# Kernel optimization log

Measured on AMD Instinct MI355X. Metric: run time of the kernel, lower is better.

Reference implementation:

```python
import jax, jax.numpy as jnp
import numpy as np

B, N, D, H = 8, 512, 1024, 16
HD = D // H
NI = 4          # num_instances == num_instances_per_batch
MAXI = 16       # max_instances
SCALE = HD ** -0.5


def _rms(t, w, eps=1e-6):
    return t * jax.lax.rsqrt(jnp.mean(t * t, axis=-1, keepdims=True) + eps) * w


def _lin(t, W, b):
    return t @ W + b


def _heads(t):
    b, n = t.shape[0], t.shape[1]
    return t.reshape(b, n, H, HD).transpose(0, 2, 1, 3)  # [b, H, n, hd]


def setup_inputs() -> dict:
    key = jax.random.key(0)
    ks = iter(jax.random.split(key, 16))

    def w(shape):
        return jax.random.normal(next(ks), shape, dtype=jnp.float32) * 0.02

    return {
        "x": jax.random.normal(next(ks), (B, N, D), dtype=jnp.float32),
        "instance_mask": jax.random.uniform(next(ks), (B, N, NI), dtype=jnp.float32),
        "Wq": w((D, D)), "bq": jnp.zeros((D,), jnp.float32),
        "Wk": w((D, D)), "bk": jnp.zeros((D,), jnp.float32),
        "Wv": w((D, D)), "bv": jnp.zeros((D,), jnp.float32),
        "Wo": w((D, D)), "bo": jnp.zeros((D,), jnp.float32),
        "Wiq": w((D, D)), "biq": jnp.zeros((D,), jnp.float32),
        "Wik": w((D, D)), "bik": jnp.zeros((D,), jnp.float32),
        "instance_embed": w((1, MAXI, D)),
        "qnorm_w": jnp.ones((HD,), jnp.float32),
        "knorm_w": jnp.ones((HD,), jnp.float32),
        "num_instances": NI,
        "num_instances_per_batch": NI,
    }


def reference(x, instance_mask, Wq, bq, Wk, bk, Wv, bv, Wo, bo,
              Wiq, biq, Wik, bik, instance_embed, qnorm_w, knorm_w,
              num_instances, num_instances_per_batch):
    # QKV projections + per-head QK-RMSNorm
    q = _rms(_heads(_lin(x, Wq, bq)), qnorm_w)   # [B,H,N,hd]
    k = _rms(_heads(_lin(x, Wk, bk)), knorm_w)
    v = _heads(_lin(x, Wv, bv))
    ni = num_instances                           # == num_instances_per_batch here,
    G = B // num_instances_per_batch             # so no leftover self-attn sub-branch;
    # (the module's initial global attention output is overwritten by this branch)
    qg = q.reshape(G, ni, H, N, HD)
    kg = k.reshape(G, ni, H, N, HD).transpose(0, 2, 1, 3, 4).reshape(G, H, ni * N, HD)
    vg = v.reshape(G, ni, H, N, HD).transpose(0, 2, 1, 3, 4).reshape(G, H, ni * N, HD)
    scores = jnp.einsum('gihnd,ghmd->gihnm', qg, kg) * SCALE  # [G,ni,H,N,ni*N]
    p = jax.nn.softmax(scores, axis=-1)
    og = jnp.einsum('gihnm,ghmd->gihnd', p, vg)
    out = og.reshape(B, H, N, HD).transpose(0, 2, 1, 3).reshape(B, N, D)
    # instance-embedding gate
    inst_feat = jnp.einsum('bnk,kd->bnd', instance_mask, instance_embed[0, :ni])
    iq = _heads(_lin(out, Wiq, biq))
    ik = _heads(_lin(inst_feat, Wik, bik))
    # mean over heads folded into the einsum (same math as mean of per-head scores)
    inst_attn = jax.nn.sigmoid(jnp.einsum('bhnd,bhmd->bnm', iq, ik) * (SCALE / H))
    gate = 1.0 + jnp.mean(inst_attn, axis=-1, keepdims=True)  # [B,N,1]
    return _lin(out * gate, Wo, bo)
```

## Files before the change

### kernel.cpp

```cpp
#include <hip/hip_runtime.h>
#include <cmath>

#define B_   8
#define N_   512
#define D_   1024
#define H_   16
#define HD_  64
#define NI_  4
#define BN_  (B_*N_)
#define KVLEN (NI_*N_)

typedef __attribute__((ext_vector_type(8)))  short  bf16x8;
typedef __attribute__((ext_vector_type(8)))  __bf16 bf16x8_t;
typedef __attribute__((ext_vector_type(16))) float  f32x16;
typedef __attribute__((ext_vector_type(4)))  short  s16x4;
typedef __attribute__((ext_vector_type(2)))  unsigned u32x2;

__device__ __forceinline__ short bf16_rn(float x) {
  unsigned u = __float_as_uint(x);
  unsigned r = (u + 0x7FFFu + ((u >> 16) & 1u)) >> 16;
  return (short)r;
}

__device__ __forceinline__ float bf2f(short x) {
  return __uint_as_float(((unsigned)(unsigned short)x) << 16);
}

__device__ __forceinline__ f32x16 mfma_bf16(bf16x8 a, bf16x8 b, f32x16 c) {
  return __builtin_amdgcn_mfma_f32_32x32x16_bf16(
      __builtin_bit_cast(bf16x8_t, a), __builtin_bit_cast(bf16x8_t, b), c, 0, 0, 0);
}

#define GLOAD16(gp, lp) __builtin_amdgcn_global_load_lds( \
  (const __attribute__((address_space(1))) unsigned*)(gp), \
  (__attribute__((address_space(3))) unsigned*)(lp), 16, 0, 0)

__device__ __forceinline__ long tiled_off(int row, int k) {
  return ((((long)(row >> 7) * 128 + (k >> 3)) * 128 + (row & 127)) * 8 + (k & 7));
}

__device__ __forceinline__ void xcd_swizzle(int& bx, int& by, int& bz) {
  const int gx = gridDim.x, gy = gridDim.y;
  const int nwg = gx * gy * gridDim.z;
  const int lin = blockIdx.x + gx * (blockIdx.y + gy * blockIdx.z);
  const int swz = (lin & 7) * (nwg >> 3) + (lin >> 3);
  bx = swz % gx;
  const int rest = swz / gx;
  by = rest % gy;
  bz = rest / gy;
}

__global__ __launch_bounds__(256) void wsplitAll(
    const float* __restrict__ Wq, const float* __restrict__ Wk,
    const float* __restrict__ Wv, const float* __restrict__ Wo,
    const float* __restrict__ x,
    short* __restrict__ QKVh, short* __restrict__ WoH,
    short* __restrict__ Xh)
{
  const int z = blockIdx.z;
  const int t  = threadIdx.x;
  if (z >= 4) {
    const int rowB = (z - 4) * 1024 + blockIdx.y * 64;
    const int colB = blockIdx.x * 64;
    const int r0 = t >> 4;
    const int c4 = t & 15;
    #pragma unroll
    for (int i = 0; i < 4; i++) {
      const int row = rowB + r0 + i * 16;
      float4 v = *(const float4*)&x[(long)row * D_ + colB + c4 * 4];
      short h[4];
      h[0] = bf16_rn(v.x);  h[1] = bf16_rn(v.y);
      h[2] = bf16_rn(v.z);  h[3] = bf16_rn(v.w);
      *(s16x4*)&Xh[tiled_off(row, colB + c4 * 4)] = *(s16x4*)h;
    }
    return;
  }
  __shared__ float tile[64][65];
  const float* W = (z == 0) ? Wq : (z == 1) ? Wk : (z == 2) ? Wv : Wo;
  const int kb = blockIdx.y * 64;
  const int cb = blockIdx.x * 64;
  const int r0 = t >> 4;
  const int c4 = t & 15;
  #pragma unroll
  for (int i = 0; i < 4; i++) {
    const int r = r0 + i * 16;
    *(float4*)&tile[r][c4 * 4] = *(const float4*)&W[(long)(kb + r) * D_ + cb + c4 * 4];
  }
  __syncthreads();
  #pragma unroll
  for (int i = 0; i < 4; i++) {
    const int c = r0 + i * 16;
    short hi[4];
    #pragma unroll
    for (int e = 0; e < 4; e++)
      hi[e] = bf16_rn(tile[c4 * 4 + e][c]);
    if (z < 3)
      *(s16x4*)&QKVh[tiled_off(z * D_ + cb + c, kb + c4 * 4)] = *(s16x4*)hi;
    else
      *(s16x4*)&WoH[tiled_off(cb + c, kb + c4 * 4)] = *(s16x4*)hi;
  }
}

__global__ __launch_bounds__(256) void fprep_p(
    const float* __restrict__ Wik, const float* __restrict__ emb,
    float* __restrict__ F4p)
{
  const int d  = blockIdx.x * 256 + threadIdx.x;
  const int eb = blockIdx.y;
  float s0 = 0, s1 = 0, s2 = 0, s3 = 0;
  for (int e = eb * 16; e < eb * 16 + 16; e++) {
    const float w = Wik[(long)e * D_ + d];
    s0 = fmaf(emb[e], w, s0);
    s1 = fmaf(emb[D_ + e], w, s1);
    s2 = fmaf(emb[2 * D_ + e], w, s2);
    s3 = fmaf(emb[3 * D_ + e], w, s3);
  }
  float* p = F4p + (long)eb * 4 * D_;
  p[d] = s0;  p[D_ + d] = s1;  p[2 * D_ + d] = s2;  p[3 * D_ + d] = s3;
}

__global__ __launch_bounds__(256) void freduce(
    const float* __restrict__ F4p, float* __restrict__ F4)
{
  const int i = blockIdx.x * 256 + threadIdx.x;
  float s = 0.f;
  #pragma unroll
  for (int eb = 0; eb < 64; eb++) s += F4p[(long)eb * 4096 + i];
  F4[i] = s;
}

__global__ __launch_bounds__(256) void hprep2(
    const float* __restrict__ Wiq, const float* __restrict__ F4,
    const float* __restrict__ bik, const float* __restrict__ biq,
    float* __restrict__ H5)
{
  __shared__ float red[4][5];
  const int t = threadIdx.x;
  const int blk = blockIdx.x;
  float s[5] = {0.f, 0.f, 0.f, 0.f, 0.f};
  const float* vr = (blk < 1024) ? Wiq + (long)blk * D_ : biq;
  for (int e = t; e < D_; e += 256) {
    const float w = vr[e];
    s[0] = fmaf(w, F4[e], s[0]);
    s[1] = fmaf(w, F4[D_ + e], s[1]);
    s[2] = fmaf(w, F4[2 * D_ + e], s[2]);
    s[3] = fmaf(w, F4[3 * D_ + e], s[3]);
    s[4] = fmaf(w, bik[e], s[4]);
  }
  #pragma unroll
  for (int j = 0; j < 5; j++)
    #pragma unroll
    for (int m = 1; m < 64; m <<= 1) s[j] += __shfl_xor(s[j], m);
  const int w64 = t >> 6, lane = t & 63;
  if (lane == 0)
    #pragma unroll
    for (int j = 0; j < 5; j++) red[w64][j] = s[j];
  __syncthreads();
  if (t < 5)
    H5[(long)blk * 5 + t] = red[0][t] + red[1][t] + red[2][t] + red[3][t];
}

template<int MODE>
__global__ __launch_bounds__(256) void mfgemm2(
    const short* __restrict__ Ahi, const short* __restrict__ Bhi,
    const float* __restrict__ b0, const float* __restrict__ b1,
    const float* __restrict__ b2,
    float* __restrict__ C, short* __restrict__ Qout,
    short* __restrict__ Kout, short* __restrict__ Vout,
    const float* __restrict__ qnw, const float* __restrict__ knw,
    int bBlk, long sC, const float* __restrict__ gate_in)
{
  __shared__ short lds[2][2][4096];
  const int t = threadIdx.x, w = t >> 6, lane = t & 63;
  int bx, by, bz;
  xcd_swizzle(bx, by, bz);
  const int rowBase = by * 128;
  const int colBase = bx * 128;
  const long aoff = (long)by * 131072;
  const long boff = (long)(bz * bBlk + bx) * 131072;

  const int op = w >> 1, half = w & 1;
  const short* mySrc = op ? Bhi + boff : Ahi + aoff;

  auto stage = [&](int buf, int tt) {
    const short* g = mySrc + ((long)tt * 512 + half * 256 + lane) * 8;
    #pragma unroll
    for (int i = 0; i < 4; i++)
      GLOAD16(g + i * 512, &lds[buf][op][(half * 256 + i * 64) * 8]);
  };

  const int wr = w >> 1, wc = w & 1;
  const int lrow = lane & 31, lk = lane >> 5;

  f32x16 acc[2][2] = {};

  auto compute = [&](int buf) {
    #pragma unroll
    for (int kh = 0; kh < 2; kh++) {
      const int kq = 2 * kh + lk;
      bf16x8 ah[2], bh[2];
      #pragma unroll
      for (int m = 0; m < 2; m++)
        ah[m] = *(const bf16x8*)&lds[buf][0][(kq * 128 + wr * 64 + m * 32 + lrow) * 8];
      #pragma unroll
      for (int n = 0; n < 2; n++)
        bh[n] = *(const bf16x8*)&lds[buf][1][(kq * 128 + wc * 64 + n * 32 + lrow) * 8];
      #pragma unroll
      for (int m = 0; m < 2; m++)
        #pragma unroll
        for (int n = 0; n < 2; n++)
          acc[m][n] = mfma_bf16(ah[m], bh[n], acc[m][n]);
    }
  };

  const int NT = 32;
  stage(0, 0);
  for (int tt = 0; tt < NT - 1; ++tt) {
    stage((tt + 1) & 1, tt + 1);
    asm volatile("s_waitcnt vmcnt(4)" ::: "memory");
    __builtin_amdgcn_s_barrier();
    __builtin_amdgcn_sched_barrier(0);
    compute(tt & 1);
    __builtin_amdgcn_s_barrier();
  }
  asm volatile("s_waitcnt vmcnt(0)" ::: "memory");
  __builtin_amdgcn_s_barrier();
  __builtin_amdgcn_sched_barrier(0);
  compute((NT - 1) & 1);

  const float* bias = (bz == 1) ? b1 : (bz == 2) ? b2 : b0;
  float bcol[2];
  #pragma unroll
  for (int n = 0; n < 2; n++)
    bcol[n] = bias[colBase + wc * 64 + n * 32 + lrow];

  if (MODE == 6 && bz == 0) {
    const float qw0 = qnw[lrow];
    const float qw1 = qnw[32 + lrow];
    const int col0 = colBase + wc * 64 + lrow;
    #pragma unroll
    for (int m = 0; m < 2; m++)
      #pragma unroll
      for (int r = 0; r < 16; r++) {
        const int row = rowBase + wr * 64 + m * 32 + (r & 3) + 8 * (r >> 2) + 4 * lk;
        const float v0 = acc[m][0][r] + bcol[0];
        const float v1 = acc[m][1][r] + bcol[1];
        float ss = v0 * v0 + v1 * v1;
        ss += __shfl_xor(ss, 1);
        ss += __shfl_xor(ss, 2);
        ss += __shfl_xor(ss, 4);
        ss += __shfl_xor(ss, 8);
        ss += __shfl_xor(ss, 16);
        const float qr = rsqrtf(ss * (1.f / 64.f) + 1e-6f) * 0.1803368801111244f;
        Qout[(long)row * D_ + col0]      = bf16_rn(v0 * qr * qw0);
        Qout[(long)row * D_ + col0 + 32] = bf16_rn(v1 * qr * qw1);
      }
    return;
  }

  if (MODE == 6 && bz == 1) {
    const float kw0 = knw[lrow];
    const float kw1 = knw[32 + lrow];
    const int h = (colBase + wc * 64) >> 6;
    #pragma unroll
    for (int m = 0; m < 2; m++)
      #pragma unroll
      for (int r = 0; r < 16; r++) {
        const int row = rowBase + wr * 64 + m * 32 + (r & 3) + 8 * (r >> 2) + 4 * lk;
        const int bb = row >> 9, g = bb >> 2;
        const int mkv = (bb & 3) * 512 + (row & 511);
        const float v0 = acc[m][0][r] + bcol[0];
        const float v1 = acc[m][1][r] + bcol[1];
        float ks2 = v0 * v0 + v1 * v1;
        ks2 += __shfl_xor(ks2, 1);
        ks2 += __shfl_xor(ks2, 2);
        ks2 += __shfl_xor(ks2, 4);
        ks2 += __shfl_xor(ks2, 8);
        ks2 += __shfl_xor(ks2, 16);
        const float kr = rsqrtf(ks2 * (1.f / 64.f) + 1e-6f);
        const long base = ((long)(g * H_ + h) * KVLEN + mkv) * 64;
        const int d0 = lrow, d1 = 32 + lrow;
        Kout[base + (((d0 >> 3) ^ (mkv & 7)) << 3) + (d0 & 7)] = bf16_rn(v0 * kr * kw0);
        Kout[base + (((d1 >> 3) ^ (mkv & 7)) << 3) + (d1 & 7)] = bf16_rn(v1 * kr * kw1);
      }
    return;
  }

  if (MODE == 6 && bz == 2) {
    #pragma unroll
    for (int m = 0; m < 2; m++)
      #pragma unroll
      for (int r = 0; r < 16; r++) {
        const int row = rowBase + wr * 64 + m * 32 + (r & 3) + 8 * (r >> 2) + 4 * lk;
        const int bb = row >> 9, g = bb >> 2;
        const int kv = (bb & 3) * 512 + (row & 511);
        const int tile = kv >> 5, vkv = kv & 31;
        #pragma unroll
        for (int n = 0; n < 2; n++) {
          const int col = colBase + wc * 64 + n * 32 + lrow;
          const int h = col >> 6, dl = col & 63;
          const long idx = ((long)(g * H_ + h) * 64 + tile) * 2048
                         + dl * 32 + (((vkv >> 3) ^ ((dl >> 1) & 3)) * 8) + (vkv & 7);
          Vout[idx] = bf16_rn(acc[m][n][r] + bcol[n]);
        }
      }
    return;
  }

  float* Cb = C + (long)bz * sC;
  #pragma unroll
  for (int m = 0; m < 2; m++) {
    #pragma unroll
    for (int r = 0; r < 16; r++) {
      const int row = rowBase + wr * 64 + m * 32 + (r & 3) + 8 * (r >> 2) + 4 * lk;
      float g = 1.f;
      if (MODE == 2) g = gate_in[row];
      #pragma unroll
      for (int n = 0; n < 2; n++) {
        const int col = colBase + wc * 64 + n * 32 + lrow;
        Cb[(long)row * D_ + col] = acc[m][n][r] * g + bcol[n];
      }
    }
  }
}

__global__ __launch_bounds__(256) void attn3(
    const short* __restrict__ q, const short* __restrict__ Knb,
    const short* __restrict__ Vtb,
    short* __restrict__ opart, float* __restrict__ lpart)
{
  int qb, h, bz;
  xcd_swizzle(qb, h, bz);
  const int b  = bz >> 1, s = bz & 1;
  const int g  = b >> 2;
  const int t  = threadIdx.x;
  const int w  = t >> 6;
  const int lane = t & 63;
  const int l31 = lane & 31, hi = lane >> 5;

  __shared__ short Kt[2][4096];
  __shared__ short Vt[2][4096];

  const int qrow = qb * 128 + w * 32 + l31;
  const short* qp = q + ((long)b * N_ + qrow) * D_ + h * HD_ + hi * 8;
  bf16x8 qf[4];
  #pragma unroll
  for (int c = 0; c < 4; c++)
    qf[c] = *(const bf16x8*)&qp[c * 16];

  const short* Kg = Knb + (long)(g * H_ + h) * KVLEN * 64 + (long)s * 32 * 2048;
  const short* Vg = Vtb + (long)(g * H_ + h) * 64 * 2048 + (long)s * 32 * 2048;

  auto stage = [&](int buf, int i) {
    GLOAD16(Kg + (long)i * 4096 + t * 8,        &Kt[buf][w * 512]);
    GLOAD16(Kg + (long)i * 4096 + 2048 + t * 8, &Kt[buf][2048 + w * 512]);
    GLOAD16(Vg + (long)i * 4096 + t * 8,        &Vt[buf][w * 512]);
    GLOAD16(Vg + (long)i * 4096 + 2048 + t * 8, &Vt[buf][2048 + w * 512]);
  };

  f32x16 oacc[2] = {};
  float l = 0.f;

  stage(0, 0);
  for (int i = 0; i < 16; ++i) {
    const int buf = i & 1;
    if (i + 1 < 16) {
      stage(buf ^ 1, i + 1);
      asm volatile("s_waitcnt vmcnt(4)" ::: "memory");
    } else {
      asm volatile("s_waitcnt vmcnt(0)" ::: "memory");
    }
    __builtin_amdgcn_s_barrier();
    __builtin_amdgcn_sched_barrier(0);

    #pragma unroll
    for (int ss = 0; ss < 2; ss++) {
      const short* Ktb = &Kt[buf][ss * 2048];
      const short* Vsb = &Vt[buf][ss * 2048];
      f32x16 sc = {};
      #pragma unroll
      for (int c = 0; c < 4; c++) {
        bf16x8 kfr = *(const bf16x8*)&Ktb[l31 * 64 + (((2 * c + hi) * 8) ^ ((l31 & 7) << 3))];
        sc = mfma_bf16(kfr, qf[c], sc);
      }
      float p[16];
      #pragma unroll
      for (int r = 0; r < 16; r++)
        p[r] = exp2f(sc[r]);
      l += ((((p[0] + p[1]) + (p[2] + p[3])) + ((p[4] + p[5]) + (p[6] + p[7])))
         + (((p[8] + p[9]) + (p[10] + p[11])) + ((p[12] + p[13]) + (p[14] + p[15]))));
      unsigned wd[8];
      #pragma unroll
      for (int i2 = 0; i2 < 8; i2++)
        asm("v_cvt_pk_bf16_f32 %0, %1, %2" : "=v"(wd[i2]) : "v"(p[2 * i2]), "v"(p[2 * i2 + 1]));
      u32x2 r0 = __builtin_amdgcn_permlane32_swap(wd[0], wd[2], false, false);
      u32x2 r1 = __builtin_amdgcn_permlane32_swap(wd[1], wd[3], false, false);
      u32x2 r2 = __builtin_amdgcn_permlane32_swap(wd[4], wd[6], false, false);
      u32x2 r3 = __builtin_amdgcn_permlane32_swap(wd[5], wd[7], false, false);
      int4 f0 = { (int)r0.x, (int)r1.x, (int)r0.y, (int)r1.y };
      int4 f1 = { (int)r2.x, (int)r3.x, (int)r2.y, (int)r3.y };
      #pragma unroll
      for (int n = 0; n < 2; n++) {
        const int d = n * 32 + l31;
        const int fd = (d >> 1) & 3;
        bf16x8 v0 = *(const bf16x8*)&Vsb[d * 32 + ((hi ^ fd) * 8)];
        bf16x8 v1 = *(const bf16x8*)&Vsb[d * 32 + (((2 | hi) ^ fd) * 8)];
        oacc[n] = mfma_bf16(__builtin_bit_cast(bf16x8, f0), v0, oacc[n]);
        oacc[n] = mfma_bf16(__builtin_bit_cast(bf16x8, f1), v1, oacc[n]);
      }
    }
    __builtin_amdgcn_s_barrier();
  }

  l += __shfl_xor(l, 32);
  #pragma unroll
  for (int r = 0; r < 16; r++) {
    const int qg = qb * 128 + w * 32 + (r & 3) + 8 * (r >> 2) + 4 * hi;
    short* op = opart + ((long)s * BN_ + b * N_ + qg) * D_ + h * HD_ + l31;
    op[0]  = bf16_rn(oacc[0][r]);
    op[32] = bf16_rn(oacc[1][r]);
  }
  if (hi == 0)
    lpart[((long)s * BN_ + b * N_ + qb * 128 + w * 32 + l31) * H_ + h] = l;
}

__global__ __launch_bounds__(256) void attn_reduce2(
    const short* __restrict__ opart, const float* __restrict__ lpart,
    const float* __restrict__ H5, const float* __restrict__ mask,
    short* __restrict__ ohi, float* __restrict__ gate)
{
  __shared__ float red[4][5];
  __shared__ float Gs[5];
  __shared__ float sred[4];
  const int t = threadIdx.x;
  const int row = blockIdx.x;
  const int bb = row >> 9;
  const int col = t * 4;
  const int h   = col >> 6;
  const float l = lpart[(long)row * H_ + h] + lpart[((long)BN_ + row) * H_ + h];
  const float inv = 1.f / l;
  s16x4 a4 = *(const s16x4*)&opart[(long)row * D_ + col];
  s16x4 b4 = *(const s16x4*)&opart[((long)BN_ + row) * D_ + col];
  float o4[4];
  #pragma unroll
  for (int c = 0; c < 4; c++)
    o4[c] = (bf2f(a4[c]) + bf2f(b4[c])) * inv;
  short hh[4];
  hh[0] = bf16_rn(o4[0]);  hh[1] = bf16_rn(o4[1]);
  hh[2] = bf16_rn(o4[2]);  hh[3] = bf16_rn(o4[3]);
  *(s16x4*)&ohi[tiled_off(row, col)] = *(s16x4*)hh;
  float s[5] = {0.f, 0.f, 0.f, 0.f, 0.f};
  #pragma unroll
  for (int cc = 0; cc < 4; cc++) {
    const float* hp = &H5[(long)(col + cc) * 5];
    #pragma unroll
    for (int j = 0; j < 5; j++) s[j] = fmaf(o4[cc], hp[j], s[j]);
  }
  #pragma unroll
  for (int j = 0; j < 5; j++)
    #pragma unroll
    for (int m = 1; m < 64; m <<= 1) s[j] += __shfl_xor(s[j], m);
  const int w64 = t >> 6, lane = t & 63;
  if (lane == 0)
    #pragma unroll
    for (int j = 0; j < 5; j++) red[w64][j] = s[j];
  __syncthreads();
  if (t < 5) Gs[t] = red[0][t] + red[1][t] + red[2][t] + red[3][t] + H5[5120 + t];
  __syncthreads();
  const float g0 = Gs[0], g1 = Gs[1], g2 = Gs[2], g3 = Gs[3], g4 = Gs[4];
  const float sc = 0.125f / 16.f;
  const float* mrow = mask + (long)bb * N_ * NI_;
  float sg = 0.f;
  #pragma unroll
  for (int q = 0; q < 2; q++) {
    const float4 mk = *(const float4*)&mrow[(t * 2 + q) * 4];
    const float z = fmaf(g0, mk.x, fmaf(g1, mk.y, fmaf(g2, mk.z, fmaf(g3, mk.w, g4))));
    sg += 1.f / (1.f + __expf(-z * sc));
  }
  #pragma unroll
  for (int m = 1; m < 64; m <<= 1) sg += __shfl_xor(sg, m);
  if (lane == 0) sred[w64] = sg;
  __syncthreads();
  if (t == 0)
    gate[row] = 1.f + (sred[0] + sred[1] + sred[2] + sred[3]) * (1.f / 512.f);
}

extern "C" void kernel_launch(void* const* d_in, const int* in_sizes, int n_in,
                              void* d_out, int out_size, void* d_ws, size_t ws_size,
                              hipStream_t stream)
{
  const float* x    = (const float*)d_in[0];
  const float* mask = (const float*)d_in[1];
  const float* Wq   = (const float*)d_in[2];
  const float* bq   = (const float*)d_in[3];
  const float* Wk   = (const float*)d_in[4];
  const float* bk   = (const float*)d_in[5];
  const float* Wv   = (const float*)d_in[6];
  const float* bv   = (const float*)d_in[7];
  const float* Wo   = (const float*)d_in[8];
  const float* bo   = (const float*)d_in[9];
  const float* Wiq  = (const float*)d_in[10];
  const float* biq  = (const float*)d_in[11];
  const float* Wik  = (const float*)d_in[12];
  const float* bik  = (const float*)d_in[13];
  const float* emb  = (const float*)d_in[14];
  const float* qnw  = (const float*)d_in[15];
  const float* knw  = (const float*)d_in[16];
  float* out = (float*)d_out;

  float* ws = (float*)d_ws;
  const size_t SZ = (size_t)BN_ * D_;
  short* Qnb  = (short*)ws;
  short* ohi  = (short*)ws;
  short* opart = (short*)(ws + SZ);
  short* Knb  = (short*)(ws + 3 * SZ);
  short* xhi  = (short*)(ws + 4 * SZ);
  short* Vtb  = xhi + SZ;
  short* Wbig_hi = (short*)(ws + 5 * SZ);
  short* Wbig_lo = Wbig_hi + (size_t)3 * D_ * D_;
  float* gate  = (float*)Wbig_hi;
  float* lpart = gate + BN_;
  short* WoH = Wbig_lo;
  float* F4  = (float*)(Wbig_lo + (size_t)D_ * D_);
  float* H5  = F4 + 4 * D_;
  float* F4p = H5 + 1025 * 5;

  const dim3 blk(256);

  fprep_p<<<dim3(4, 64), blk, 0, stream>>>(Wik, emb, F4p);
  freduce<<<dim3(16), blk, 0, stream>>>(F4p, F4);
  hprep2<<<dim3(1025), blk, 0, stream>>>(Wiq, F4, bik, biq, H5);

  wsplitAll<<<dim3(16, 16, 8), blk, 0, stream>>>(
      Wq, Wk, Wv, Wo, x, Wbig_hi, WoH, xhi);

  mfgemm2<6><<<dim3(8, 32, 3), blk, 0, stream>>>(
      xhi, Wbig_hi, bq, bk, bv,
      nullptr, Qnb, Knb, Vtb, qnw, knw, 8, 0, nullptr);

  attn3<<<dim3(N_ / 128, H_, B_ * 2), blk, 0, stream>>>(
      Qnb, Knb, Vtb, opart, lpart);

  attn_reduce2<<<BN_, blk, 0, stream>>>(opart, lpart, H5, mask, ohi, gate);

  mfgemm2<2><<<dim3(8, 32, 1), blk, 0, stream>>>(
      ohi, WoH, bo, nullptr, nullptr,
      out, nullptr, nullptr, nullptr, nullptr, nullptr, 0, 0, gate);
}
```

Before: 174.1 us.

## Fold Wik prep into wsplit launch and use 128x64 tiles for output GEMM

Merges the fprep_p kernel into the wsplitAll launch as an extra z-slice, removing one kernel launch and letting the small reduction overlap with the weight conversion. Replaces the templated output projection with a dedicated GEMM that uses 128x64 tiles, giving 512 blocks instead of 256 to fill more of the device's CUs. The narrower tile lowers per-block data reuse, and only one wave stages the B tile, which may limit load bandwidth.

Result: no change. 175.1 us (+0.6%).

```diff
diff --git a/kernel.cpp b/kernel.cpp
--- a/kernel.cpp
+++ b/kernel.cpp
@@ -54,11 +54,28 @@
     const float* __restrict__ Wq, const float* __restrict__ Wk,
     const float* __restrict__ Wv, const float* __restrict__ Wo,
     const float* __restrict__ x,
+    const float* __restrict__ Wik, const float* __restrict__ emb,
     short* __restrict__ QKVh, short* __restrict__ WoH,
-    short* __restrict__ Xh)
+    short* __restrict__ Xh, float* __restrict__ F4p)
 {
   const int z = blockIdx.z;
   const int t  = threadIdx.x;
+  if (z == 8) {
+    const int fid = blockIdx.y * 16 + blockIdx.x;
+    const int d  = (fid & 3) * 256 + t;
+    const int eb = fid >> 2;
+    float s0 = 0, s1 = 0, s2 = 0, s3 = 0;
+    for (int e = eb * 16; e < eb * 16 + 16; e++) {
+      const float w = Wik[(long)e * D_ + d];
+      s0 = fmaf(emb[e], w, s0);
+      s1 = fmaf(emb[D_ + e], w, s1);
+      s2 = fmaf(emb[2 * D_ + e], w, s2);
+      s3 = fmaf(emb[3 * D_ + e], w, s3);
+    }
+    float* p = F4p + (long)eb * 4 * D_;
+    p[d] = s0;  p[D_ + d] = s1;  p[2 * D_ + d] = s2;  p[3 * D_ + d] = s3;
+    return;
+  }
   if (z >= 4) {
     const int rowB = (z - 4) * 1024 + blockIdx.y * 64;
     const int colB = blockIdx.x * 64;
@@ -99,24 +116,6 @@
     else
       *(s16x4*)&WoH[tiled_off(cb + c, kb + c4 * 4)] = *(s16x4*)hi;
   }
-}
-
-__global__ __launch_bounds__(256) void fprep_p(
-    const float* __restrict__ Wik, const float* __restrict__ emb,
-    float* __restrict__ F4p)
-{
-  const int d  = blockIdx.x * 256 + threadIdx.x;
-  const int eb = blockIdx.y;
-  float s0 = 0, s1 = 0, s2 = 0, s3 = 0;
-  for (int e = eb * 16; e < eb * 16 + 16; e++) {
-    const float w = Wik[(long)e * D_ + d];
-    s0 = fmaf(emb[e], w, s0);
-    s1 = fmaf(emb[D_ + e], w, s1);
-    s2 = fmaf(emb[2 * D_ + e], w, s2);
-    s3 = fmaf(emb[3 * D_ + e], w, s3);
-  }
-  float* p = F4p + (long)eb * 4 * D_;
-  p[d] = s0;  p[D_ + d] = s1;  p[2 * D_ + d] = s2;  p[3 * D_ + d] = s3;
 }
 
 __global__ __launch_bounds__(256) void freduce(
@@ -160,15 +159,13 @@
     H5[(long)blk * 5 + t] = red[0][t] + red[1][t] + red[2][t] + red[3][t];
 }
 
-template<int MODE>
-__global__ __launch_bounds__(256) void mfgemm2(
+__global__ __launch_bounds__(256) void mfgemmQKV(
     const short* __restrict__ Ahi, const short* __restrict__ Bhi,
     const float* __restrict__ b0, const float* __restrict__ b1,
     const float* __restrict__ b2,
-    float* __restrict__ C, short* __restrict__ Qout,
-    short* __restrict__ Kout, short* __restrict__ Vout,
-    const float* __restrict__ qnw, const float* __restrict__ knw,
-    int bBlk, long sC, const float* __restrict__ gate_in)
+    short* __restrict__ Qout, short* __restrict__ Kout,
+    short* __restrict__ Vout,
+    const float* __restrict__ qnw, const float* __restrict__ knw)
 {
   __shared__ short lds[2][2][4096];
   const int t = threadIdx.x, w = t >> 6, lane = t & 63;
@@ -177,7 +174,7 @@
   const int rowBase = by * 128;
   const int colBase = bx * 128;
   const long aoff = (long)by * 131072;
-  const long boff = (long)(bz * bBlk + bx) * 131072;
+  const long boff = (long)(bz * 8 + bx) * 131072;
 
   const int op = w >> 1, half = w & 1;
   const short* mySrc = op ? Bhi + boff : Ahi + aoff;
@@ -234,7 +231,7 @@
   for (int n = 0; n < 2; n++)
     bcol[n] = bias[colBase + wc * 64 + n * 32 + lrow];
 
-  if (MODE == 6 && bz == 0) {
+  if (bz == 0) {
     const float qw0 = qnw[lrow];
     const float qw1 = qnw[32 + lrow];
     const int col0 = colBase + wc * 64 + lrow;
@@ -258,7 +255,7 @@
     return;
   }
 
-  if (MODE == 6 && bz == 1) {
+  if (bz == 1) {
     const float kw0 = knw[lrow];
     const float kw1 = knw[32 + lrow];
     const int h = (colBase + wc * 64) >> 6;
@@ -286,42 +283,96 @@
     return;
   }
 
-  if (MODE == 6 && bz == 2) {
-    #pragma unroll
-    for (int m = 0; m < 2; m++)
-      #pragma unroll
-      for (int r = 0; r < 16; r++) {
-        const int row = rowBase + wr * 64 + m * 32 + (r & 3) + 8 * (r >> 2) + 4 * lk;
-        const int bb = row >> 9, g = bb >> 2;
-        const int kv = (bb & 3) * 512 + (row & 511);
-        const int tile = kv >> 5, vkv = kv & 31;
-        #pragma unroll
-        for (int n = 0; n < 2; n++) {
-          const int col = colBase + wc * 64 + n * 32 + lrow;
-          const int h = col >> 6, dl = col & 63;
-          const long idx = ((long)(g * H_ + h) * 64 + tile) * 2048
-                         + dl * 32 + (((vkv >> 3) ^ ((dl >> 1) & 3)) * 8) + (vkv & 7);
-          Vout[idx] = bf16_rn(acc[m][n][r] + bcol[n]);
-        }
-      }
-    return;
-  }
-
-  float* Cb = C + (long)bz * sC;
-  #pragma unroll
-  for (int m = 0; m < 2; m++) {
+  #pragma unroll
+  for (int m = 0; m < 2; m++)
     #pragma unroll
     for (int r = 0; r < 16; r++) {
       const int row = rowBase + wr * 64 + m * 32 + (r & 3) + 8 * (r >> 2) + 4 * lk;
-      float g = 1.f;
-      if (MODE == 2) g = gate_in[row];
+      const int bb = row >> 9, g = bb >> 2;
+      const int kv = (bb & 3) * 512 + (row & 511);
+      const int tile = kv >> 5, vkv = kv & 31;
       #pragma unroll
       for (int n = 0; n < 2; n++) {
         const int col = colBase + wc * 64 + n * 32 + lrow;
-        Cb[(long)row * D_ + col] = acc[m][n][r] * g + bcol[n];
+        const int h = col >> 6, dl = col & 63;
+        const long idx = ((long)(g * H_ + h) * 64 + tile) * 2048
+                       + dl * 32 + (((vkv >> 3) ^ ((dl >> 1) & 3)) * 8) + (vkv & 7);
+        Vout[idx] = bf16_rn(acc[m][n][r] + bcol[n]);
       }
     }
-  }
+}
+
+__global__ __launch_bounds__(256) void mfgemmF(
+    const short* __restrict__ Ahi, const short* __restrict__ Bhi,
+    const float* __restrict__ bo, float* __restrict__ C,
+    const float* __restrict__ gate_in)
+{
+  __shared__ short As[2][4096];
+  __shared__ short Bs[2][2048];
+  const int t = threadIdx.x, w = t >> 6, lane = t & 63;
+  int bx, by, bz;
+  xcd_swizzle(bx, by, bz);
+  const int rowBase = by * 128;
+  const int colBase = bx * 64;
+  const long aoff = (long)by * 131072;
+
+  auto stage = [&](int buf, int tt) {
+    if (w < 2) {
+      const short* g = Ahi + aoff + ((long)tt * 512 + w * 256 + lane) * 8;
+      #pragma unroll
+      for (int i = 0; i < 4; i++)
+        GLOAD16(g + i * 512, &As[buf][(w * 256 + i * 64) * 8]);
+    } else if (w == 2) {
+      const short* g = Bhi + ((long)(bx >> 1) * 128 + (long)tt * 4) * 1024
+                     + (bx & 1) * 512 + lane * 8;
+      #pragma unroll
+      for (int i = 0; i < 4; i++)
+        GLOAD16(g + i * 1024, &Bs[buf][i * 512]);
+    }
+  };
+
+  const int wr = w >> 1, wc = w & 1;
+  const int lrow = lane & 31, lk = lane >> 5;
+
+  f32x16 acc[2] = {};
+
+  auto compute = [&](int buf) {
+    #pragma unroll
+    for (int kh = 0; kh < 2; kh++) {
+      const int kq = 2 * kh + lk;
+      bf16x8 bh = *(const bf16x8*)&Bs[buf][(kq * 64 + wc * 32 + lrow) * 8];
+      #pragma unroll
+      for (int m = 0; m < 2; m++) {
+        bf16x8 ah = *(const bf16x8*)&As[buf][(kq * 128 + wr * 64 + m * 32 + lrow) * 8];
+        acc[m] = mfma_bf16(ah, bh, acc[m]);
+      }
+    }
+  };
+
+  const int NT = 32;
+  stage(0, 0);
+  for (int tt = 0; tt < NT - 1; ++tt) {
+    stage((tt + 1) & 1, tt + 1);
+    asm volatile("s_waitcnt vmcnt(4)" ::: "memory");
+    __builtin_amdgcn_s_barrier();
+    __builtin_amdgcn_sched_barrier(0);
+    compute(tt & 1);
+    __builtin_amdgcn_s_barrier();
+  }
+  asm volatile("s_waitcnt vmcnt(0)" ::: "memory");
+  __builtin_amdgcn_s_barrier();
+  __builtin_amdgcn_sched_barrier(0);
+  compute((NT - 1) & 1);
+
+  const int col = colBase + wc * 32 + lrow;
+  const float bc = bo[col];
+  #pragma unroll
+  for (int m = 0; m < 2; m++)
+    #pragma unroll
+    for (int r = 0; r < 16; r++) {
+      const int row = rowBase + wr * 64 + m * 32 + (r & 3) + 8 * (r >> 2) + 4 * lk;
+      C[(long)row * D_ + col] = acc[m][r] * gate_in[row] + bc;
+    }
 }
 
 __global__ __launch_bounds__(256) void attn3(
@@ -527,23 +578,19 @@
 
   const dim3 blk(256);
 
-  fprep_p<<<dim3(4, 64), blk, 0, stream>>>(Wik, emb, F4p);
+  wsplitAll<<<dim3(16, 16, 9), blk, 0, stream>>>(
+      Wq, Wk, Wv, Wo, x, Wik, emb, Wbig_hi, WoH, xhi, F4p);
+
   freduce<<<dim3(16), blk, 0, stream>>>(F4p, F4);
   hprep2<<<dim3(1025), blk, 0, stream>>>(Wiq, F4, bik, biq, H5);
 
-  wsplitAll<<<dim3(16, 16, 8), blk, 0, stream>>>(
-      Wq, Wk, Wv, Wo, x, Wbig_hi, WoH, xhi);
-
-  mfgemm2<6><<<dim3(8, 32, 3), blk, 0, stream>>>(
-      xhi, Wbig_hi, bq, bk, bv,
-      nullptr, Qnb, Knb, Vtb, qnw, knw, 8, 0, nullptr);
+  mfgemmQKV<<<dim3(8, 32, 3), blk, 0, stream>>>(
+      xhi, Wbig_hi, bq, bk, bv, Qnb, Knb, Vtb, qnw, knw);
 
   attn3<<<dim3(N_ / 128, H_, B_ * 2), blk, 0, stream>>>(
       Qnb, Knb, Vtb, opart, lpart);
 
   attn_reduce2<<<BN_, blk, 0, stream>>>(opart, lpart, H5, mask, ohi, gate);
 
-  mfgemm2<2><<<dim3(8, 32, 1), blk, 0, stream>>>(
-      ohi, WoH, bo, nullptr, nullptr,
-      out, nullptr, nullptr, nullptr, nullptr, nullptr, 0, 0, gate);
-}
+  mfgemmF<<<dim3(16, 32), blk, 0, stream>>>(ohi, WoH, bo, out, gate);
+}
```
